# Optimization experiments

Hardware: AMD Instinct MI355X
Metric: run time of the kernel (lower is better)

The kernel has to match this reference:

```python
import jax, jax.numpy as jnp
import numpy as np

EPS = 1e-5
N_LANG = 5

def _ln(x, gamma, beta):
    mu = jnp.mean(x, axis=-1, keepdims=True)
    var = jnp.mean((x - mu) ** 2, axis=-1, keepdims=True)
    return (x - mu) * jax.lax.rsqrt(var + EPS) * gamma + beta

def setup_inputs() -> dict:
    key = jax.random.key(0)
    ks = jax.random.split(key, 20)
    B, S, E, T, H = 16, 512, 768, 768, 1024
    s = lambda fan_in: 1.0 / np.sqrt(fan_in)
    inp = {
        'ner_features': jax.random.normal(ks[0], (B, S, E), jnp.float32),
        'topic_features': jax.random.normal(ks[1], (B, S, T), jnp.float32),
        'language_ids': jax.random.randint(ks[2], (B,), 0, N_LANG, jnp.int64),
        # ner transform: Linear(E,H) + LayerNorm(H)
        'W_ner': jax.random.uniform(ks[3], (E, H), jnp.float32, -s(E), s(E)),
        'b_ner': jnp.zeros((H,), jnp.float32),
        'g_ner': jnp.ones((H,), jnp.float32),
        'be_ner': jnp.zeros((H,), jnp.float32),
        # topic transform: Linear(T,H) + LayerNorm(H)
        'W_top': jax.random.uniform(ks[4], (T, H), jnp.float32, -s(T), s(T)),
        'b_top': jnp.zeros((H,), jnp.float32),
        'g_top': jnp.ones((H,), jnp.float32),
        'be_top': jnp.zeros((H,), jnp.float32),
        # 5 language gate networks, stacked on leading lang axis
        'Wg1': jax.random.uniform(ks[5], (N_LANG, 2 * H, H), jnp.float32, -s(2 * H), s(2 * H)),
        'bg1': jnp.zeros((N_LANG, H), jnp.float32),
        'gg': jnp.ones((N_LANG, H), jnp.float32),
        'bg': jnp.zeros((N_LANG, H), jnp.float32),
        'Wg2': jax.random.uniform(ks[6], (N_LANG, H, 2), jnp.float32, -s(H), s(H)),
        'bg2': jnp.zeros((N_LANG, 2), jnp.float32),
    }
    return inp

def reference(ner_features, topic_features, language_ids,
              W_ner, b_ner, g_ner, be_ner,
              W_top, b_top, g_top, be_top,
              Wg1, bg1, gg, bg, Wg2, bg2):
    # shared transforms: [B,S,H]
    ner_t = jax.nn.relu(_ln(ner_features @ W_ner + b_ner, g_ner, be_ner))
    top_t = jax.nn.relu(_ln(topic_features @ W_top + b_top, g_top, be_top))
    combined = jnp.concatenate([ner_t, top_t], axis=-1)  # [B,S,2H]
    # all-language gate MLPs (faithful to the original redundant compute)
    h = jnp.einsum('bsd,ldh->lbsh', combined, Wg1) + bg1[:, None, None, :]
    h = jax.nn.relu(_ln(h, gg[:, None, None, :], bg[:, None, None, :]))
    gates_all = jax.nn.sigmoid(jnp.einsum('lbsh,lhk->lbsk', h, Wg2) + bg2[:, None, None, :])  # [L,B,S,2]
    mask = (language_ids[None, :] == jnp.arange(N_LANG)[:, None]).astype(gates_all.dtype)  # [L,B]
    gates = jnp.einsum('lb,lbsk->bsk', mask, gates_all)  # [B,S,2]
    gated_ner = ner_t * gates[..., 0:1]
    gated_topic = top_t * gates[..., 1:2]
    # dropout in eval mode (identity) for determinism
    return gated_ner, gated_topic
```

## Files before the change

kernel.cpp:

```cpp
#include <hip/hip_runtime.h>

typedef __attribute__((ext_vector_type(8))) short short8;
typedef __attribute__((ext_vector_type(4))) float f32x4;

__device__ __forceinline__ float bf2f(unsigned short u) {
    union { unsigned int i; float f; } v; v.i = ((unsigned int)u) << 16; return v.f;
}
__device__ __forceinline__ unsigned short f2bf(float f) {
    union { float f; unsigned int i; } v; v.f = f;
    unsigned int r = v.i + 0x7fffu + ((v.i >> 16) & 1u);
    return (unsigned short)(r >> 16);
}
__device__ __forceinline__ void gload16(const unsigned short* g, unsigned short* l) {
    __builtin_amdgcn_global_load_lds(
        (const __attribute__((address_space(1))) unsigned int*)g,
        (__attribute__((address_space(3))) unsigned int*)l, 16, 0, 0);
}

template<int K, int MODE>
__global__ __launch_bounds__(256) void gemm_p2(
    const unsigned short* __restrict__ A,
    const unsigned short* __restrict__ Bta,
    const unsigned short* __restrict__ Btb,
    const float* __restrict__ biasa,
    const float* __restrict__ biasb,
    unsigned short* __restrict__ Cb,
    const int* __restrict__ lang)
{
    __shared__ __align__(16) unsigned short As0[128][64], Bs0[128][64];
    __shared__ __align__(16) unsigned short As1[128][64], Bs1[128][64];

    const int t = threadIdx.x;
    const int nwg = gridDim.x * gridDim.y;
    const int bid = blockIdx.y * gridDim.x + blockIdx.x;
    const int swz = (bid & 7) * (nwg >> 3) + (bid >> 3);
    const int gm0 = (swz >> 3) * 128;
    const int gn0 = (swz & 7) * 128;

    const unsigned short* Bt;
    const float* bias;
    int sel = 0;
    if (MODE == 0) {
        sel = gm0 >> 13;
        Bt = sel ? Btb : Bta;
        bias = sel ? biasb : biasa;
    } else {
        const int l = lang[gm0 >> 9];
        Bt = Bta + (size_t)l * (K * 1024);
        bias = biasa + l * 1024;
    }

    const int lane = t & 63;
    const int w = t >> 6, wm = w >> 1, wn = w & 1;
    const int fr = lane & 15, g4 = lane >> 4, f7 = lane & 7;
    const int csw0 = ((0 + g4) ^ f7) * 8;
    const int csw1 = ((4 + g4) ^ f7) * 8;

    const int srow = t >> 3;
    const int swcol = ((t & 7) ^ (srow & 7)) * 8;
    const int lcol = (t & 7) * 8;
    const unsigned short* ag = A  + (size_t)(gm0 + srow) * K + swcol;
    const unsigned short* bg = Bt + (size_t)(gn0 + srow) * K + swcol;

    f32x4 acc[4][4];
#pragma unroll
    for (int m = 0; m < 4; ++m)
#pragma unroll
        for (int n = 0; n < 4; ++n)
            acc[m][n] = (f32x4){0.f, 0.f, 0.f, 0.f};

    auto stage = [&](unsigned short (*As)[64], unsigned short (*Bs)[64], int k0) {
#pragma unroll
        for (int i = 0; i < 4; ++i) {
            gload16(ag + (size_t)(i * 32) * K + k0, &As[i * 32 + srow][lcol]);
            gload16(bg + (size_t)(i * 32) * K + k0, &Bs[i * 32 + srow][lcol]);
        }
    };
    auto compute = [&](const unsigned short (*As)[64], const unsigned short (*Bs)[64]) {
        short8 a0[4], b0[4];
#pragma unroll
        for (int m = 0; m < 4; ++m) a0[m] = *(const short8*)&As[wm * 64 + m * 16 + fr][csw0];
#pragma unroll
        for (int n = 0; n < 4; ++n) b0[n] = *(const short8*)&Bs[wn * 64 + n * 16 + fr][csw0];
#pragma unroll
        for (int m = 0; m < 4; ++m)
#pragma unroll
            for (int n = 0; n < 4; ++n)
                acc[m][n] = __builtin_amdgcn_mfma_f32_16x16x32_bf16(a0[m], b0[n], acc[m][n], 0, 0, 0);
#pragma unroll
        for (int m = 0; m < 4; ++m) a0[m] = *(const short8*)&As[wm * 64 + m * 16 + fr][csw1];
#pragma unroll
        for (int n = 0; n < 4; ++n) b0[n] = *(const short8*)&Bs[wn * 64 + n * 16 + fr][csw1];
#pragma unroll
        for (int m = 0; m < 4; ++m)
#pragma unroll
            for (int n = 0; n < 4; ++n)
                acc[m][n] = __builtin_amdgcn_mfma_f32_16x16x32_bf16(a0[m], b0[n], acc[m][n], 0, 0, 0);
    };

    constexpr int NT = K / 64;
    stage(As0, Bs0, 0);
    stage(As1, Bs1, 64);

    for (int tt = 0; tt < NT; tt += 2) {
        asm volatile("s_waitcnt vmcnt(8)" ::: "memory");
        __builtin_amdgcn_s_barrier();
        asm volatile("" ::: "memory");
        __builtin_amdgcn_sched_barrier(0);
        compute(As0, Bs0);
        __builtin_amdgcn_sched_barrier(0);
        __builtin_amdgcn_s_barrier();
        if (tt + 2 < NT) stage(As0, Bs0, (tt + 2) * 64);
        if (tt + 2 < NT) asm volatile("s_waitcnt vmcnt(8)" ::: "memory");
        else             asm volatile("s_waitcnt vmcnt(0)" ::: "memory");
        __builtin_amdgcn_s_barrier();
        asm volatile("" ::: "memory");
        __builtin_amdgcn_sched_barrier(0);
        compute(As1, Bs1);
        __builtin_amdgcn_sched_barrier(0);
        __builtin_amdgcn_s_barrier();
        if (tt + 3 < NT) stage(As1, Bs1, (tt + 3) * 64);
    }

    const int fq = lane >> 4;
    const size_t pitch  = (MODE == 0) ? 2048 : 1024;
    const size_t coloff = (MODE == 0) ? (size_t)sel * 1024 : 0;
    const int rbase = (MODE == 0) ? (gm0 & 8191) : gm0;
#pragma unroll
    for (int n = 0; n < 4; ++n) {
        const int col = gn0 + wn * 64 + n * 16 + fr;
        const float bv = bias[col];
#pragma unroll
        for (int m = 0; m < 4; ++m) {
            const int row0 = rbase + wm * 64 + m * 16 + fq * 4;
#pragma unroll
            for (int r = 0; r < 4; ++r)
                Cb[(size_t)(row0 + r) * pitch + coloff + col] = f2bf(acc[m][n][r] + bv);
        }
    }
}

__global__ __launch_bounds__(256) void wt_bf16(
    const float* __restrict__ W, unsigned short* __restrict__ Wt, int K, int N)
{
    __shared__ float tile[32][33];
    W  += (size_t)blockIdx.z * K * N;
    Wt += (size_t)blockIdx.z * K * N;
    const int n0 = blockIdx.x * 32, k0 = blockIdx.y * 32;
    const int x = threadIdx.x & 31, y = threadIdx.x >> 5;
#pragma unroll
    for (int i = 0; i < 4; ++i)
        tile[y + 8 * i][x] = W[(size_t)(k0 + y + 8 * i) * N + n0 + x];
    __syncthreads();
#pragma unroll
    for (int i = 0; i < 4; ++i)
        Wt[(size_t)(n0 + y + 8 * i) * K + k0 + x] = f2bf(tile[x][y + 8 * i]);
}

__global__ __launch_bounds__(256) void conv_bf16(
    const float* __restrict__ in, unsigned short* __restrict__ out)
{
    const size_t i = ((size_t)blockIdx.x * 256 + threadIdx.x) * 8;
    const float4 a = ((const float4*)(in + i))[0];
    const float4 b = ((const float4*)(in + i))[1];
    ushort4 u, v;
    u.x = f2bf(a.x); u.y = f2bf(a.y); u.z = f2bf(a.z); u.w = f2bf(a.w);
    v.x = f2bf(b.x); v.y = f2bf(b.y); v.z = f2bf(b.z); v.w = f2bf(b.w);
    *(ushort4*)(out + i)     = u;
    *(ushort4*)(out + i + 4) = v;
}

__global__ __launch_bounds__(256) void ln_relu_c(
    unsigned short* __restrict__ comb,
    const float* __restrict__ gn, const float* __restrict__ bn,
    const float* __restrict__ gt, const float* __restrict__ btp)
{
    const int b = blockIdx.x, t = threadIdx.x;
    const int r = b >> 1, half = b & 1;
    unsigned short* p = comb + (size_t)r * 2048 + half * 1024 + t * 4;
    ushort4 u = *(const ushort4*)p;
    const float x0 = bf2f(u.x), x1 = bf2f(u.y), x2 = bf2f(u.z), x3 = bf2f(u.w);
    float s1 = x0 + x1 + x2 + x3;
    float s2 = x0 * x0 + x1 * x1 + x2 * x2 + x3 * x3;
#pragma unroll
    for (int off = 32; off > 0; off >>= 1) {
        s1 += __shfl_down(s1, off);
        s2 += __shfl_down(s2, off);
    }
    __shared__ float red[8];
    const int wid = t >> 6;
    if ((t & 63) == 0) { red[wid] = s1; red[4 + wid] = s2; }
    __syncthreads();
    s1 = red[0] + red[1] + red[2] + red[3];
    s2 = red[4] + red[5] + red[6] + red[7];
    const float mean = s1 * (1.0f / 1024.0f);
    const float var = fmaxf(s2 * (1.0f / 1024.0f) - mean * mean, 0.0f);
    const float rstd = rsqrtf(var + 1e-5f);
    const float* G  = half ? gt : gn;
    const float* Be = half ? btp : bn;
    const float4 g  = ((const float4*)G)[t];
    const float4 be = ((const float4*)Be)[t];
    u.x = f2bf(fmaxf((x0 - mean) * rstd * g.x + be.x, 0.0f));
    u.y = f2bf(fmaxf((x1 - mean) * rstd * g.y + be.y, 0.0f));
    u.z = f2bf(fmaxf((x2 - mean) * rstd * g.z + be.z, 0.0f));
    u.w = f2bf(fmaxf((x3 - mean) * rstd * g.w + be.w, 0.0f));
    *(ushort4*)p = u;
}

__global__ __launch_bounds__(256) void ln_relu_l(
    const unsigned short* __restrict__ in, unsigned short* __restrict__ out,
    const float* __restrict__ gg, const float* __restrict__ bg,
    const int* __restrict__ lang)
{
    const int r = blockIdx.x, t = threadIdx.x;
    const ushort4 u = *(const ushort4*)(in + (size_t)r * 1024 + t * 4);
    const float x0 = bf2f(u.x), x1 = bf2f(u.y), x2 = bf2f(u.z), x3 = bf2f(u.w);
    float s1 = x0 + x1 + x2 + x3;
    float s2 = x0 * x0 + x1 * x1 + x2 * x2 + x3 * x3;
#pragma unroll
    for (int off = 32; off > 0; off >>= 1) {
        s1 += __shfl_down(s1, off);
        s2 += __shfl_down(s2, off);
    }
    __shared__ float red[8];
    const int wid = t >> 6;
    if ((t & 63) == 0) { red[wid] = s1; red[4 + wid] = s2; }
    __syncthreads();
    s1 = red[0] + red[1] + red[2] + red[3];
    s2 = red[4] + red[5] + red[6] + red[7];
    const float mean = s1 * (1.0f / 1024.0f);
    const float var = fmaxf(s2 * (1.0f / 1024.0f) - mean * mean, 0.0f);
    const float rstd = rsqrtf(var + 1e-5f);
    const int l = lang[r >> 9];
    const float4 g  = ((const float4*)(gg + l * 1024))[t];
    const float4 be = ((const float4*)(bg + l * 1024))[t];
    ushort4 h;
    h.x = f2bf(fmaxf((x0 - mean) * rstd * g.x + be.x, 0.0f));
    h.y = f2bf(fmaxf((x1 - mean) * rstd * g.y + be.y, 0.0f));
    h.z = f2bf(fmaxf((x2 - mean) * rstd * g.z + be.z, 0.0f));
    h.w = f2bf(fmaxf((x3 - mean) * rstd * g.w + be.w, 0.0f));
    *(ushort4*)(out + (size_t)r * 1024 + t * 4) = h;
}

__global__ __launch_bounds__(256) void gate_scale(
    const unsigned short* __restrict__ h, const unsigned short* __restrict__ comb,
    const float* __restrict__ Wg2, const float* __restrict__ bg2,
    const int* __restrict__ lang, float* __restrict__ outN, float* __restrict__ outT)
{
    const int r = blockIdx.x, t = threadIdx.x;
    const int l = lang[r >> 9];
    const ushort4 hv = *(const ushort4*)(h + (size_t)r * 1024 + t * 4);
    const float4* W = (const float4*)(Wg2 + (size_t)l * 2048);
    const float4 wa = W[t * 2], wb = W[t * 2 + 1];
    const float h0 = bf2f(hv.x), h1 = bf2f(hv.y), h2 = bf2f(hv.z), h3 = bf2f(hv.w);
    float d0 = h0 * wa.x + h1 * wa.z + h2 * wb.x + h3 * wb.z;
    float d1 = h0 * wa.y + h1 * wa.w + h2 * wb.y + h3 * wb.w;
#pragma unroll
    for (int off = 32; off > 0; off >>= 1) {
        d0 += __shfl_down(d0, off);
        d1 += __shfl_down(d1, off);
    }
    __shared__ float red[8];
    const int wid = t >> 6;
    if ((t & 63) == 0) { red[wid] = d0; red[4 + wid] = d1; }
    __syncthreads();
    d0 = red[0] + red[1] + red[2] + red[3] + bg2[l * 2 + 0];
    d1 = red[4] + red[5] + red[6] + red[7] + bg2[l * 2 + 1];
    const float g0 = 1.0f / (1.0f + __expf(-d0));
    const float g1 = 1.0f / (1.0f + __expf(-d1));
    const ushort4 cn = *(const ushort4*)(comb + (size_t)r * 2048 + t * 4);
    const ushort4 ct = *(const ushort4*)(comb + (size_t)r * 2048 + 1024 + t * 4);
    float4 a, b;
    a.x = bf2f(cn.x) * g0; a.y = bf2f(cn.y) * g0; a.z = bf2f(cn.z) * g0; a.w = bf2f(cn.w) * g0;
    b.x = bf2f(ct.x) * g1; b.y = bf2f(ct.y) * g1; b.z = bf2f(ct.z) * g1; b.w = bf2f(ct.w) * g1;
    ((float4*)(outN + (size_t)r * 1024))[t] = a;
    ((float4*)(outT + (size_t)r * 1024))[t] = b;
}

extern "C" void kernel_launch(void* const* d_in, const int* in_sizes, int n_in,
                              void* d_out, int out_size, void* d_ws, size_t ws_size,
                              hipStream_t stream)
{
    const float* ner    = (const float*)d_in[0];
    const float* top    = (const float*)d_in[1];
    const int*   lang   = (const int*)d_in[2];
    const float* W_ner  = (const float*)d_in[3];
    const float* b_ner  = (const float*)d_in[4];
    const float* g_ner  = (const float*)d_in[5];
    const float* be_ner = (const float*)d_in[6];
    const float* W_top  = (const float*)d_in[7];
    const float* b_top  = (const float*)d_in[8];
    const float* g_top  = (const float*)d_in[9];
    const float* be_top = (const float*)d_in[10];
    const float* Wg1    = (const float*)d_in[11];
    const float* bg1    = (const float*)d_in[12];
    const float* gg     = (const float*)d_in[13];
    const float* bgb    = (const float*)d_in[14];
    const float* Wg2    = (const float*)d_in[15];
    const float* bg2    = (const float*)d_in[16];

    float* out  = (float*)d_out;
    float* outN = out;
    float* outT = out + 8388608;

    char* ws = (char*)d_ws;
    unsigned short* combined = (unsigned short*)ws;
    unsigned short* actb     = (unsigned short*)(ws + 33554432);
    unsigned short* hbuf     = (unsigned short*)(ws + 33554432);
    unsigned short* Wg1t     = (unsigned short*)(ws + 58720256);
    unsigned short* W_nert   = (unsigned short*)outT;
    unsigned short* W_topt   = W_nert + 786432;
    unsigned short* preln2   = (unsigned short*)outN;

    wt_bf16<<<dim3(32, 24, 1), 256, 0, stream>>>(W_ner, W_nert, 768, 1024);
    wt_bf16<<<dim3(32, 24, 1), 256, 0, stream>>>(W_top, W_topt, 768, 1024);
    wt_bf16<<<dim3(32, 64, 5), 256, 0, stream>>>(Wg1, Wg1t, 2048, 1024);

    conv_bf16<<<3072, 256, 0, stream>>>(ner, actb);
    conv_bf16<<<3072, 256, 0, stream>>>(top, actb + 6291456);

    gemm_p2<768, 0><<<dim3(8, 128), 256, 0, stream>>>(
        actb, W_nert, W_topt, b_ner, b_top, combined, nullptr);
    ln_relu_c<<<16384, 256, 0, stream>>>(combined, g_ner, be_ner, g_top, be_top);

    gemm_p2<2048, 1><<<dim3(8, 64), 256, 0, stream>>>(
        combined, Wg1t, nullptr, bg1, nullptr, preln2, lang);
    ln_relu_l<<<8192, 256, 0, stream>>>(preln2, hbuf, gg, bgb, lang);

    gate_scale<<<8192, 256, 0, stream>>>(hbuf, combined, Wg2, bg2, lang, outN, outT);
}
```

Measured before the change: 149.8 us.

## Enlarge GEMM tiles to 512-thread blocks and fuse gate LayerNorm with gating

The GEMM kernel now uses 512-thread workgroups with 256-row tiles: 256x256 for the first projection GEMM and 256x128 for the gate GEMM. It also switches to a single-tile-per-iteration double-buffered loop with B fragments held in registers, and raises wave priority around the MFMA bursts. The aim is more operand reuse per LDS load and fewer workgroups. Separately, the language LayerNorm+ReLU kernel is fused with the gate/scale kernel, which removes one launch and the write-then-read of the hidden buffer, and the pre-LN buffer moves into workspace. Larger tiles raise register and LDS pressure (64KB+ LDS per block), and 256 blocks may leave some CUs underused.

```diff
diff --git a/kernel.cpp b/kernel.cpp
--- a/kernel.cpp
+++ b/kernel.cpp
@@ -18,7 +18,7 @@
 }
 
 template<int K, int MODE>
-__global__ __launch_bounds__(256) void gemm_p2(
+__global__ __launch_bounds__(512, 2) void gemm8(
     const unsigned short* __restrict__ A,
     const unsigned short* __restrict__ Bta,
     const unsigned short* __restrict__ Btb,
@@ -27,15 +27,23 @@
     unsigned short* __restrict__ Cb,
     const int* __restrict__ lang)
 {
-    __shared__ __align__(16) unsigned short As0[128][64], Bs0[128][64];
-    __shared__ __align__(16) unsigned short As1[128][64], Bs1[128][64];
+    constexpr int BN  = (MODE == 0) ? 256 : 128;
+    constexpr int MR  = (MODE == 0) ? 8 : 4;
+    constexpr int MPC = MR / 4;
+    constexpr int NBLK = 1024 / BN;
+    constexpr int LPT = 4 + BN / 64;
+    constexpr int NT  = K / 64;
+
+    __shared__ __align__(16) unsigned short As[2][256][64];
+    __shared__ __align__(16) unsigned short Bs[2][BN][64];
 
     const int t = threadIdx.x;
-    const int nwg = gridDim.x * gridDim.y;
-    const int bid = blockIdx.y * gridDim.x + blockIdx.x;
+    const int nwg = gridDim.x;
+    const int bid = blockIdx.x;
     const int swz = (bid & 7) * (nwg >> 3) + (bid >> 3);
-    const int gm0 = (swz >> 3) * 128;
-    const int gn0 = (swz & 7) * 128;
+    const int mb = swz / NBLK;
+    const int nb = swz % NBLK;
+    const int gm0 = mb * 256, gn0 = nb * BN;
 
     const unsigned short* Bt;
     const float* bias;
@@ -46,80 +54,79 @@
         bias = sel ? biasb : biasa;
     } else {
         const int l = lang[gm0 >> 9];
-        Bt = Bta + (size_t)l * (K * 1024);
+        Bt = Bta + (size_t)l * ((size_t)K * 1024);
         bias = biasa + l * 1024;
     }
 
-    const int lane = t & 63;
-    const int w = t >> 6, wm = w >> 1, wn = w & 1;
+    const int lane = t & 63, w = t >> 6;
+    const int wm = (MODE == 0) ? (w >> 2) : (w >> 1);
+    const int wn = (MODE == 0) ? (w & 3) : (w & 1);
     const int fr = lane & 15, g4 = lane >> 4, f7 = lane & 7;
-    const int csw0 = ((0 + g4) ^ f7) * 8;
-    const int csw1 = ((4 + g4) ^ f7) * 8;
-
-    const int srow = t >> 3;
-    const int swcol = ((t & 7) ^ (srow & 7)) * 8;
-    const int lcol = (t & 7) * 8;
-    const unsigned short* ag = A  + (size_t)(gm0 + srow) * K + swcol;
-    const unsigned short* bg = Bt + (size_t)(gn0 + srow) * K + swcol;
-
-    f32x4 acc[4][4];
-#pragma unroll
-    for (int m = 0; m < 4; ++m)
+
+    const int sr  = t >> 3;
+    const int gsw = ((t & 7) ^ (sr & 7)) * 8;
+    const int lc  = (t & 7) * 8;
+    const unsigned short* ag = A  + (size_t)(gm0 + sr) * K + gsw;
+    const unsigned short* bg = Bt + (size_t)(gn0 + sr) * K + gsw;
+
+    f32x4 acc[MR][4];
+#pragma unroll
+    for (int m = 0; m < MR; ++m)
 #pragma unroll
         for (int n = 0; n < 4; ++n)
             acc[m][n] = (f32x4){0.f, 0.f, 0.f, 0.f};
 
-    auto stage = [&](unsigned short (*As)[64], unsigned short (*Bs)[64], int k0) {
-#pragma unroll
-        for (int i = 0; i < 4; ++i) {
-            gload16(ag + (size_t)(i * 32) * K + k0, &As[i * 32 + srow][lcol]);
-            gload16(bg + (size_t)(i * 32) * K + k0, &Bs[i * 32 + srow][lcol]);
-        }
+    auto stage = [&](int buf, int k0) {
+#pragma unroll
+        for (int i = 0; i < 4; ++i)
+            gload16(ag + (size_t)(i * 64) * K + k0, &As[buf][i * 64 + sr][lc]);
+#pragma unroll
+        for (int i = 0; i < BN / 64; ++i)
+            gload16(bg + (size_t)(i * 64) * K + k0, &Bs[buf][i * 64 + sr][lc]);
     };
-    auto compute = [&](const unsigned short (*As)[64], const unsigned short (*Bs)[64]) {
-        short8 a0[4], b0[4];
-#pragma unroll
-        for (int m = 0; m < 4; ++m) a0[m] = *(const short8*)&As[wm * 64 + m * 16 + fr][csw0];
-#pragma unroll
-        for (int n = 0; n < 4; ++n) b0[n] = *(const short8*)&Bs[wn * 64 + n * 16 + fr][csw0];
-#pragma unroll
-        for (int m = 0; m < 4; ++m)
-#pragma unroll
-            for (int n = 0; n < 4; ++n)
-                acc[m][n] = __builtin_amdgcn_mfma_f32_16x16x32_bf16(a0[m], b0[n], acc[m][n], 0, 0, 0);
-#pragma unroll
-        for (int m = 0; m < 4; ++m) a0[m] = *(const short8*)&As[wm * 64 + m * 16 + fr][csw1];
-#pragma unroll
-        for (int n = 0; n < 4; ++n) b0[n] = *(const short8*)&Bs[wn * 64 + n * 16 + fr][csw1];
-#pragma unroll
-        for (int m = 0; m < 4; ++m)
-#pragma unroll
-            for (int n = 0; n < 4; ++n)
-                acc[m][n] = __builtin_amdgcn_mfma_f32_16x16x32_bf16(a0[m], b0[n], acc[m][n], 0, 0, 0);
-    };
-
-    constexpr int NT = K / 64;
-    stage(As0, Bs0, 0);
-    stage(As1, Bs1, 64);
-
-    for (int tt = 0; tt < NT; tt += 2) {
-        asm volatile("s_waitcnt vmcnt(8)" ::: "memory");
-        __builtin_amdgcn_s_barrier();
-        asm volatile("" ::: "memory");
-        __builtin_amdgcn_sched_barrier(0);
-        compute(As0, Bs0);
-        __builtin_amdgcn_sched_barrier(0);
-        __builtin_amdgcn_s_barrier();
-        if (tt + 2 < NT) stage(As0, Bs0, (tt + 2) * 64);
-        if (tt + 2 < NT) asm volatile("s_waitcnt vmcnt(8)" ::: "memory");
+
+    stage(0, 0);
+    if (NT > 1) stage(1, 64);
+
+    for (int tt = 0; tt < NT; ++tt) {
+        const int cur = tt & 1;
+        if (tt + 1 < NT) asm volatile("s_waitcnt vmcnt(%0)" :: "i"(LPT) : "memory");
         else             asm volatile("s_waitcnt vmcnt(0)" ::: "memory");
         __builtin_amdgcn_s_barrier();
         asm volatile("" ::: "memory");
         __builtin_amdgcn_sched_barrier(0);
-        compute(As1, Bs1);
+
+        short8 bf_[4][2];
+#pragma unroll
+        for (int n = 0; n < 4; ++n)
+#pragma unroll
+            for (int kk = 0; kk < 2; ++kk)
+                bf_[n][kk] = *(const short8*)&Bs[cur][wn * 64 + n * 16 + fr][((kk * 4 + g4) ^ f7) * 8];
+
+#pragma unroll
+        for (int c = 0; c < 4; ++c) {
+            short8 af_[MPC][2];
+#pragma unroll
+            for (int mm = 0; mm < MPC; ++mm)
+#pragma unroll
+                for (int kk = 0; kk < 2; ++kk)
+                    af_[mm][kk] = *(const short8*)&As[cur][wm * (MR * 16) + (c * MPC + mm) * 16 + fr][((kk * 4 + g4) ^ f7) * 8];
+            __builtin_amdgcn_s_setprio(1);
+#pragma unroll
+            for (int mm = 0; mm < MPC; ++mm)
+#pragma unroll
+                for (int n = 0; n < 4; ++n)
+#pragma unroll
+                    for (int kk = 0; kk < 2; ++kk)
+                        acc[c * MPC + mm][n] = __builtin_amdgcn_mfma_f32_16x16x32_bf16(
+                            af_[mm][kk], bf_[n][kk], acc[c * MPC + mm][n], 0, 0, 0);
+            __builtin_amdgcn_s_setprio(0);
+        }
+
         __builtin_amdgcn_sched_barrier(0);
         __builtin_amdgcn_s_barrier();
-        if (tt + 3 < NT) stage(As1, Bs1, (tt + 3) * 64);
+        asm volatile("" ::: "memory");
+        if (tt + 2 < NT) stage(cur, (tt + 2) * 64);
     }
 
     const int fq = lane >> 4;
@@ -131,8 +138,8 @@
         const int col = gn0 + wn * 64 + n * 16 + fr;
         const float bv = bias[col];
 #pragma unroll
-        for (int m = 0; m < 4; ++m) {
-            const int row0 = rbase + wm * 64 + m * 16 + fq * 4;
+        for (int m = 0; m < MR; ++m) {
+            const int row0 = rbase + wm * (MR * 16) + m * 16 + fq * 4;
 #pragma unroll
             for (int r = 0; r < 4; ++r)
                 Cb[(size_t)(row0 + r) * pitch + coloff + col] = f2bf(acc[m][n][r] + bv);
@@ -207,13 +214,16 @@
     *(ushort4*)p = u;
 }
 
-__global__ __launch_bounds__(256) void ln_relu_l(
-    const unsigned short* __restrict__ in, unsigned short* __restrict__ out,
-    const float* __restrict__ gg, const float* __restrict__ bg,
-    const int* __restrict__ lang)
+__global__ __launch_bounds__(256) void ln_gate(
+    const unsigned short* __restrict__ preln, const unsigned short* __restrict__ comb,
+    const float* __restrict__ gg, const float* __restrict__ bgb,
+    const float* __restrict__ Wg2, const float* __restrict__ bg2,
+    const int* __restrict__ lang,
+    float* __restrict__ outN, float* __restrict__ outT)
 {
     const int r = blockIdx.x, t = threadIdx.x;
-    const ushort4 u = *(const ushort4*)(in + (size_t)r * 1024 + t * 4);
+    const int l = lang[r >> 9];
+    const ushort4 u = *(const ushort4*)(preln + (size_t)r * 1024 + t * 4);
     const float x0 = bf2f(u.x), x1 = bf2f(u.y), x2 = bf2f(u.z), x3 = bf2f(u.w);
     float s1 = x0 + x1 + x2 + x3;
     float s2 = x0 * x0 + x1 * x1 + x2 * x2 + x3 * x3;
@@ -231,28 +241,14 @@
     const float mean = s1 * (1.0f / 1024.0f);
     const float var = fmaxf(s2 * (1.0f / 1024.0f) - mean * mean, 0.0f);
     const float rstd = rsqrtf(var + 1e-5f);
-    const int l = lang[r >> 9];
     const float4 g  = ((const float4*)(gg + l * 1024))[t];
-    const float4 be = ((const float4*)(bg + l * 1024))[t];
-    ushort4 h;
-    h.x = f2bf(fmaxf((x0 - mean) * rstd * g.x + be.x, 0.0f));
-    h.y = f2bf(fmaxf((x1 - mean) * rstd * g.y + be.y, 0.0f));
-    h.z = f2bf(fmaxf((x2 - mean) * rstd * g.z + be.z, 0.0f));
-    h.w = f2bf(fmaxf((x3 - mean) * rstd * g.w + be.w, 0.0f));
-    *(ushort4*)(out + (size_t)r * 1024 + t * 4) = h;
-}
-
-__global__ __launch_bounds__(256) void gate_scale(
-    const unsigned short* __restrict__ h, const unsigned short* __restrict__ comb,
-    const float* __restrict__ Wg2, const float* __restrict__ bg2,
-    const int* __restrict__ lang, float* __restrict__ outN, float* __restrict__ outT)
-{
-    const int r = blockIdx.x, t = threadIdx.x;
-    const int l = lang[r >> 9];
-    const ushort4 hv = *(const ushort4*)(h + (size_t)r * 1024 + t * 4);
+    const float4 be = ((const float4*)(bgb + l * 1024))[t];
+    const float h0 = fmaxf((x0 - mean) * rstd * g.x + be.x, 0.0f);
+    const float h1 = fmaxf((x1 - mean) * rstd * g.y + be.y, 0.0f);
+    const float h2 = fmaxf((x2 - mean) * rstd * g.z + be.z, 0.0f);
+    const float h3 = fmaxf((x3 - mean) * rstd * g.w + be.w, 0.0f);
     const float4* W = (const float4*)(Wg2 + (size_t)l * 2048);
     const float4 wa = W[t * 2], wb = W[t * 2 + 1];
-    const float h0 = bf2f(hv.x), h1 = bf2f(hv.y), h2 = bf2f(hv.z), h3 = bf2f(hv.w);
     float d0 = h0 * wa.x + h1 * wa.z + h2 * wb.x + h3 * wb.z;
     float d1 = h0 * wa.y + h1 * wa.w + h2 * wb.y + h3 * wb.w;
 #pragma unroll
@@ -260,8 +256,7 @@
         d0 += __shfl_down(d0, off);
         d1 += __shfl_down(d1, off);
     }
-    __shared__ float red[8];
-    const int wid = t >> 6;
+    __syncthreads();
     if ((t & 63) == 0) { red[wid] = d0; red[4 + wid] = d1; }
     __syncthreads();
     d0 = red[0] + red[1] + red[2] + red[3] + bg2[l * 2 + 0];
@@ -306,11 +301,10 @@
     char* ws = (char*)d_ws;
     unsigned short* combined = (unsigned short*)ws;
     unsigned short* actb     = (unsigned short*)(ws + 33554432);
-    unsigned short* hbuf     = (unsigned short*)(ws + 33554432);
+    unsigned short* preln2   = (unsigned short*)(ws + 33554432);
     unsigned short* Wg1t     = (unsigned short*)(ws + 58720256);
     unsigned short* W_nert   = (unsigned short*)outT;
     unsigned short* W_topt   = W_nert + 786432;
-    unsigned short* preln2   = (unsigned short*)outN;
 
     wt_bf16<<<dim3(32, 24, 1), 256, 0, stream>>>(W_ner, W_nert, 768, 1024);
     wt_bf16<<<dim3(32, 24, 1), 256, 0, stream>>>(W_top, W_topt, 768, 1024);
@@ -319,13 +313,12 @@
     conv_bf16<<<3072, 256, 0, stream>>>(ner, actb);
     conv_bf16<<<3072, 256, 0, stream>>>(top, actb + 6291456);
 
-    gemm_p2<768, 0><<<dim3(8, 128), 256, 0, stream>>>(
+    gemm8<768, 0><<<256, 512, 0, stream>>>(
         actb, W_nert, W_topt, b_ner, b_top, combined, nullptr);
     ln_relu_c<<<16384, 256, 0, stream>>>(combined, g_ner, be_ner, g_top, be_top);
 
-    gemm_p2<2048, 1><<<dim3(8, 64), 256, 0, stream>>>(
+    gemm8<2048, 1><<<256, 512, 0, stream>>>(
         combined, Wg1t, nullptr, bg1, nullptr, preln2, lang);
-    ln_relu_l<<<8192, 256, 0, stream>>>(preln2, hbuf, gg, bgb, lang);
-
-    gate_scale<<<8192, 256, 0, stream>>>(hbuf, combined, Wg2, bg2, lang, outN, outT);
-}
+
+    ln_gate<<<8192, 256, 0, stream>>>(preln2, combined, gg, bgb, Wg2, bg2, lang, outN, outT);
+}
```

After: 152.3 us. About the same (+1.6%).

## Fuse prep kernels into one launch and merge gate LayerNorm with gating

Applied to the files above, without the earlier changes.

Five weight-transpose and activation-conversion launches are merged into a single prep_all kernel that dispatches on block index. The second LayerNorm+ReLU is fused into the gate/scale kernel, so the bf16 hidden buffer is never written to or read back from global memory, and the pre-LN buffer moves into the workspace. This cuts launch overhead and one full intermediate round trip, at the cost of an extra barrier for reusing the shared reduction buffer and a heterogeneous prep kernel.

```diff
diff --git a/kernel.cpp b/kernel.cpp
--- a/kernel.cpp
+++ b/kernel.cpp
@@ -18,7 +18,7 @@
 }
 
 template<int K, int MODE>
-__global__ __launch_bounds__(256) void gemm_p2(
+__global__ __launch_bounds__(256) void gemm_r3(
     const unsigned short* __restrict__ A,
     const unsigned short* __restrict__ Bta,
     const unsigned short* __restrict__ Btb,
@@ -31,9 +31,10 @@
     __shared__ __align__(16) unsigned short As1[128][64], Bs1[128][64];
 
     const int t = threadIdx.x;
-    const int nwg = gridDim.x * gridDim.y;
-    const int bid = blockIdx.y * gridDim.x + blockIdx.x;
-    const int swz = (bid & 7) * (nwg >> 3) + (bid >> 3);
+    const int nx = gridDim.x;
+    const int bid = blockIdx.y * nx + blockIdx.x;
+    const int cpx = (nx * gridDim.y) >> 3;
+    const int swz = (bid & 7) * cpx + (bid >> 3);
     const int gm0 = (swz >> 3) * 128;
     const int gn0 = (swz & 7) * 128;
 
@@ -46,7 +47,7 @@
         bias = sel ? biasb : biasa;
     } else {
         const int l = lang[gm0 >> 9];
-        Bt = Bta + (size_t)l * (K * 1024);
+        Bt = Bta + (size_t)l * ((size_t)K * 1024);
         bias = biasa + l * 1024;
     }
 
@@ -140,14 +141,12 @@
     }
 }
 
-__global__ __launch_bounds__(256) void wt_bf16(
-    const float* __restrict__ W, unsigned short* __restrict__ Wt, int K, int N)
-{
-    __shared__ float tile[32][33];
-    W  += (size_t)blockIdx.z * K * N;
-    Wt += (size_t)blockIdx.z * K * N;
-    const int n0 = blockIdx.x * 32, k0 = blockIdx.y * 32;
-    const int x = threadIdx.x & 31, y = threadIdx.x >> 5;
+__device__ __forceinline__ void wt_tile(
+    const float* W, unsigned short* Wt, int K, int N, int bx, int by,
+    float (*tile)[33], int t)
+{
+    const int n0 = bx * 32, k0 = by * 32;
+    const int x = t & 31, y = t >> 5;
 #pragma unroll
     for (int i = 0; i < 4; ++i)
         tile[y + 8 * i][x] = W[(size_t)(k0 + y + 8 * i) * N + n0 + x];
@@ -156,18 +155,43 @@
     for (int i = 0; i < 4; ++i)
         Wt[(size_t)(n0 + y + 8 * i) * K + k0 + x] = f2bf(tile[x][y + 8 * i]);
 }
-
-__global__ __launch_bounds__(256) void conv_bf16(
-    const float* __restrict__ in, unsigned short* __restrict__ out)
-{
-    const size_t i = ((size_t)blockIdx.x * 256 + threadIdx.x) * 8;
+__device__ __forceinline__ void conv_chunk(
+    const float* in, unsigned short* out, int b, int t)
+{
+    const size_t i = ((size_t)b * 256 + t) * 8;
     const float4 a = ((const float4*)(in + i))[0];
-    const float4 b = ((const float4*)(in + i))[1];
+    const float4 c = ((const float4*)(in + i))[1];
     ushort4 u, v;
     u.x = f2bf(a.x); u.y = f2bf(a.y); u.z = f2bf(a.z); u.w = f2bf(a.w);
-    v.x = f2bf(b.x); v.y = f2bf(b.y); v.z = f2bf(b.z); v.w = f2bf(b.w);
+    v.x = f2bf(c.x); v.y = f2bf(c.y); v.z = f2bf(c.z); v.w = f2bf(c.w);
     *(ushort4*)(out + i)     = u;
     *(ushort4*)(out + i + 4) = v;
+}
+
+__global__ __launch_bounds__(256) void prep_all(
+    const float* __restrict__ W_ner, unsigned short* __restrict__ W_nert,
+    const float* __restrict__ W_top, unsigned short* __restrict__ W_topt,
+    const float* __restrict__ Wg1,   unsigned short* __restrict__ Wg1t,
+    const float* __restrict__ ner,   const float* __restrict__ top,
+    unsigned short* __restrict__ actb)
+{
+    __shared__ float tile[32][33];
+    int b = blockIdx.x;
+    const int t = threadIdx.x;
+    if (b < 768)  { wt_tile(W_ner, W_nert, 768, 1024, b % 32, b / 32, tile, t); return; }
+    b -= 768;
+    if (b < 768)  { wt_tile(W_top, W_topt, 768, 1024, b % 32, b / 32, tile, t); return; }
+    b -= 768;
+    if (b < 10240) {
+        const int z = b / 2048, r = b % 2048;
+        wt_tile(Wg1 + (size_t)z * 2097152, Wg1t + (size_t)z * 2097152,
+                2048, 1024, r % 32, r / 32, tile, t);
+        return;
+    }
+    b -= 10240;
+    if (b < 3072) { conv_chunk(ner, actb, b, t); return; }
+    b -= 3072;
+    conv_chunk(top, actb + 6291456, b, t);
 }
 
 __global__ __launch_bounds__(256) void ln_relu_c(
@@ -207,13 +231,16 @@
     *(ushort4*)p = u;
 }
 
-__global__ __launch_bounds__(256) void ln_relu_l(
-    const unsigned short* __restrict__ in, unsigned short* __restrict__ out,
-    const float* __restrict__ gg, const float* __restrict__ bg,
-    const int* __restrict__ lang)
+__global__ __launch_bounds__(256) void ln_gate(
+    const unsigned short* __restrict__ preln, const unsigned short* __restrict__ comb,
+    const float* __restrict__ gg, const float* __restrict__ bgb,
+    const float* __restrict__ Wg2, const float* __restrict__ bg2,
+    const int* __restrict__ lang,
+    float* __restrict__ outN, float* __restrict__ outT)
 {
     const int r = blockIdx.x, t = threadIdx.x;
-    const ushort4 u = *(const ushort4*)(in + (size_t)r * 1024 + t * 4);
+    const int l = lang[r >> 9];
+    const ushort4 u = *(const ushort4*)(preln + (size_t)r * 1024 + t * 4);
     const float x0 = bf2f(u.x), x1 = bf2f(u.y), x2 = bf2f(u.z), x3 = bf2f(u.w);
     float s1 = x0 + x1 + x2 + x3;
     float s2 = x0 * x0 + x1 * x1 + x2 * x2 + x3 * x3;
@@ -231,28 +258,14 @@
     const float mean = s1 * (1.0f / 1024.0f);
     const float var = fmaxf(s2 * (1.0f / 1024.0f) - mean * mean, 0.0f);
     const float rstd = rsqrtf(var + 1e-5f);
-    const int l = lang[r >> 9];
     const float4 g  = ((const float4*)(gg + l * 1024))[t];
-    const float4 be = ((const float4*)(bg + l * 1024))[t];
-    ushort4 h;
-    h.x = f2bf(fmaxf((x0 - mean) * rstd * g.x + be.x, 0.0f));
-    h.y = f2bf(fmaxf((x1 - mean) * rstd * g.y + be.y, 0.0f));
-    h.z = f2bf(fmaxf((x2 - mean) * rstd * g.z + be.z, 0.0f));
-    h.w = f2bf(fmaxf((x3 - mean) * rstd * g.w + be.w, 0.0f));
-    *(ushort4*)(out + (size_t)r * 1024 + t * 4) = h;
-}
-
-__global__ __launch_bounds__(256) void gate_scale(
-    const unsigned short* __restrict__ h, const unsigned short* __restrict__ comb,
-    const float* __restrict__ Wg2, const float* __restrict__ bg2,
-    const int* __restrict__ lang, float* __restrict__ outN, float* __restrict__ outT)
-{
-    const int r = blockIdx.x, t = threadIdx.x;
-    const int l = lang[r >> 9];
-    const ushort4 hv = *(const ushort4*)(h + (size_t)r * 1024 + t * 4);
+    const float4 be = ((const float4*)(bgb + l * 1024))[t];
+    const float h0 = fmaxf((x0 - mean) * rstd * g.x + be.x, 0.0f);
+    const float h1 = fmaxf((x1 - mean) * rstd * g.y + be.y, 0.0f);
+    const float h2 = fmaxf((x2 - mean) * rstd * g.z + be.z, 0.0f);
+    const float h3 = fmaxf((x3 - mean) * rstd * g.w + be.w, 0.0f);
     const float4* W = (const float4*)(Wg2 + (size_t)l * 2048);
     const float4 wa = W[t * 2], wb = W[t * 2 + 1];
-    const float h0 = bf2f(hv.x), h1 = bf2f(hv.y), h2 = bf2f(hv.z), h3 = bf2f(hv.w);
     float d0 = h0 * wa.x + h1 * wa.z + h2 * wb.x + h3 * wb.z;
     float d1 = h0 * wa.y + h1 * wa.w + h2 * wb.y + h3 * wb.w;
 #pragma unroll
@@ -260,8 +273,7 @@
         d0 += __shfl_down(d0, off);
         d1 += __shfl_down(d1, off);
     }
-    __shared__ float red[8];
-    const int wid = t >> 6;
+    __syncthreads();
     if ((t & 63) == 0) { red[wid] = d0; red[4 + wid] = d1; }
     __syncthreads();
     d0 = red[0] + red[1] + red[2] + red[3] + bg2[l * 2 + 0];
@@ -306,26 +318,20 @@
     char* ws = (char*)d_ws;
     unsigned short* combined = (unsigned short*)ws;
     unsigned short* actb     = (unsigned short*)(ws + 33554432);
-    unsigned short* hbuf     = (unsigned short*)(ws + 33554432);
+    unsigned short* preln2   = (unsigned short*)(ws + 33554432);
     unsigned short* Wg1t     = (unsigned short*)(ws + 58720256);
     unsigned short* W_nert   = (unsigned short*)outT;
     unsigned short* W_topt   = W_nert + 786432;
-    unsigned short* preln2   = (unsigned short*)outN;
-
-    wt_bf16<<<dim3(32, 24, 1), 256, 0, stream>>>(W_ner, W_nert, 768, 1024);
-    wt_bf16<<<dim3(32, 24, 1), 256, 0, stream>>>(W_top, W_topt, 768, 1024);
-    wt_bf16<<<dim3(32, 64, 5), 256, 0, stream>>>(Wg1, Wg1t, 2048, 1024);
-
-    conv_bf16<<<3072, 256, 0, stream>>>(ner, actb);
-    conv_bf16<<<3072, 256, 0, stream>>>(top, actb + 6291456);
-
-    gemm_p2<768, 0><<<dim3(8, 128), 256, 0, stream>>>(
+
+    prep_all<<<17920, 256, 0, stream>>>(W_ner, W_nert, W_top, W_topt,
+                                        Wg1, Wg1t, ner, top, actb);
+
+    gemm_r3<768, 0><<<dim3(8, 128), 256, 0, stream>>>(
         actb, W_nert, W_topt, b_ner, b_top, combined, nullptr);
     ln_relu_c<<<16384, 256, 0, stream>>>(combined, g_ner, be_ner, g_top, be_top);
 
-    gemm_p2<2048, 1><<<dim3(8, 64), 256, 0, stream>>>(
+    gemm_r3<2048, 1><<<dim3(8, 64), 256, 0, stream>>>(
         combined, Wg1t, nullptr, bg1, nullptr, preln2, lang);
-    ln_relu_l<<<8192, 256, 0, stream>>>(preln2, hbuf, gg, bgb, lang);
-
-    gate_scale<<<8192, 256, 0, stream>>>(hbuf, combined, Wg2, bg2, lang, outN, outT);
-}
+
+    ln_gate<<<8192, 256, 0, stream>>>(preln2, combined, gg, bgb, Wg2, bg2, lang, outN, outT);
+}
```

After: 139.9 us. 1.07x faster.
